# Performance work log

Hardware: AMD Instinct MI355X
Metric: run time of the kernel (lower is better)

Reference implementation:

```python
import jax, jax.numpy as jnp
import numpy as np

NUM_HEADS = 24
EPS = 1e-6


def rms_norm(x, scale):
    # fp32 RMSNorm over last dim, matching torch F.rms_norm(eps=1e-6)
    xf = x.astype(jnp.float32)
    rrms = jax.lax.rsqrt(jnp.mean(xf * xf, axis=-1, keepdims=True) + EPS)
    return (xf * rrms * scale.astype(jnp.float32)).astype(x.dtype)


def rope_rotate(x, pe):
    # x: [B,H,L,D]; pe: [B,1,L,D/2,2,2] rotation matrices
    B, H, L, D = x.shape
    xr = x.astype(jnp.float32).reshape(B, H, L, D // 2, 1, 2)
    out = pe[..., 0] * xr[..., 0] + pe[..., 1] * xr[..., 1]  # [B,H,L,D/2,2]
    return out.reshape(B, H, L, D).astype(x.dtype)


def setup_inputs() -> dict:
    key = jax.random.key(0)
    ks = jax.random.split(key, 6)
    B, L, C = 1, 2048, 3072
    H = NUM_HEADS
    D = C // H
    x = jax.random.normal(ks[0], (B, L, C), dtype=jnp.float32)
    # pe: proper RoPE rotation matrices [[cos,-sin],[sin,cos]] -> [B,1,L,D/2,2,2]
    theta = jax.random.uniform(ks[1], (B, 1, L, D // 2), dtype=jnp.float32) * (2.0 * np.pi)
    cos, sin = jnp.cos(theta), jnp.sin(theta)
    row0 = jnp.stack([cos, -sin], axis=-1)
    row1 = jnp.stack([sin, cos], axis=-1)
    pe = jnp.stack([row0, row1], axis=-2)  # [B,1,L,D/2,2,2]
    w_qkv = jax.random.normal(ks[2], (3 * C, C), dtype=jnp.float32) * (1.0 / np.sqrt(C))
    q_scale = jnp.ones((D,), dtype=jnp.float32)
    k_scale = jnp.ones((D,), dtype=jnp.float32)
    w_proj = jax.random.normal(ks[3], (C, C), dtype=jnp.float32) * (1.0 / np.sqrt(C))
    b_proj = jnp.zeros((C,), dtype=jnp.float32)
    return {"x": x, "pe": pe, "w_qkv": w_qkv, "q_scale": q_scale,
            "k_scale": k_scale, "w_proj": w_proj, "b_proj": b_proj}


def reference(x, pe, w_qkv, q_scale, k_scale, w_proj, b_proj):
    B, L, C = x.shape
    H = NUM_HEADS
    D = C // H
    qkv = x @ w_qkv.T                                   # [B,L,3C]
    qkv = qkv.reshape(B, L, 3, H, D).transpose(2, 0, 3, 1, 4)  # [3,B,H,L,D]
    q, k, v = qkv[0], qkv[1], qkv[2]
    q = rms_norm(q, q_scale)
    k = rms_norm(k, k_scale)
    q = rope_rotate(q, pe)
    k = rope_rotate(k, pe)
    scale = 1.0 / np.sqrt(D)
    scores = jnp.einsum('bhqd,bhkd->bhqk', q, k) * jnp.asarray(scale, q.dtype)
    attn = jax.nn.softmax(scores, axis=-1)
    out = jnp.einsum('bhqk,bhkd->bhqd', attn, v)        # [B,H,L,D]
    out = out.transpose(0, 2, 1, 3).reshape(B, L, C)    # [B,L,C]
    return out @ w_proj.T + b_proj
```

## Files before the change

### kernel.cpp

```cpp
#include <hip/hip_runtime.h>

typedef __attribute__((ext_vector_type(8))) __bf16 bf16x8;
typedef __attribute__((ext_vector_type(4))) float f32x4;

typedef __attribute__((address_space(1))) void gvoid;
typedef __attribute__((address_space(3))) void lvoid;

__device__ __forceinline__ float bf2f(unsigned int u) {
    union { unsigned int u; float f; } v; v.u = u << 16; return v.f;
}
__device__ __forceinline__ unsigned short f2bf(float f) {
    union { float f; unsigned int u; } v; v.f = f;
    unsigned int r = v.u + 0x7fffu + ((v.u >> 16) & 1u);
    return (unsigned short)(r >> 16);
}
__device__ __forceinline__ unsigned int pack2(float a, float b) {
    return (unsigned int)f2bf(a) | ((unsigned int)f2bf(b) << 16);
}
__device__ __forceinline__ void async16(const void* g, void* l) {
    __builtin_amdgcn_global_load_lds((gvoid*)g, (lvoid*)l, 16, 0, 0);
}
__device__ __forceinline__ float exp2f_hw(float x) {
    return __builtin_amdgcn_exp2f(x);
}


__global__ __launch_bounds__(256)
void cvt_bf16(const float4* __restrict__ s, uint4* __restrict__ d, int n8) {
    int i = blockIdx.x * 256 + threadIdx.x;
    if (i >= n8) return;
    float4 a = s[2 * i], b = s[2 * i + 1];
    uint4 o;
    o.x = pack2(a.x, a.y); o.y = pack2(a.z, a.w);
    o.z = pack2(b.x, b.y); o.w = pack2(b.z, b.w);
    d[i] = o;
}

#define GEMM_CORE(A_, lda_, B_, ldb_, K_)                                        \
    __shared__ __align__(16) unsigned short As[4][4096];                         \
    __shared__ __align__(16) unsigned short Bs[4][4096];                         \
    const int t = threadIdx.x, lane = t & 63;                                    \
    const int wm = t >> 7, wn = (t >> 6) & 1;                                    \
    const int lr = lane & 15, kc = lane >> 4;                                    \
    const int NK = (K_) / 32;                                                    \
    const int e0 = t * 8, e1 = (256 + t) * 8;                                    \
    const int r0 = e0 >> 5, c0 = (e0 >> 3) & 3;                                  \
    const int r1 = e1 >> 5, c1 = (e1 >> 3) & 3;                                  \
    const int g0 = (c0 ^ ((r0 >> 1) & 3)) * 8;                                   \
    const int g1 = (c1 ^ ((r1 >> 1) & 3)) * 8;                                   \
    const unsigned short* Ag0 = &(A_)[(size_t)(m0 + r0) * (lda_) + g0];          \
    const unsigned short* Ag1 = &(A_)[(size_t)(m0 + r1) * (lda_) + g1];          \
    const unsigned short* Bg0 = &(B_)[(size_t)(n0 + r0) * (ldb_) + g0];          \
    const unsigned short* Bg1 = &(B_)[(size_t)(n0 + r1) * (ldb_) + g1];          \
    f32x4 acc[4][4] = {};                                                        \
    RSTAGE(0) RSTAGE(1) RSTAGE(2)                                                \
    asm volatile("s_waitcnt vmcnt(8)" ::: "memory");                             \
    __builtin_amdgcn_s_barrier();                                                \
    for (int kt = 0; kt < NK; ++kt) {                                            \
        const int sl = kt & 3;                                                   \
        bf16x8 af[4], bfr[4];                                                    \
        _Pragma("unroll")                                                        \
        for (int i = 0; i < 4; ++i) {                                            \
            int ra = wm * 64 + i * 16 + lr;                                      \
            int rb = wn * 64 + i * 16 + lr;                                      \
            af[i]  = *(const bf16x8*)&As[sl][ra * 32 + ((kc ^ ((ra >> 1) & 3)) * 8)]; \
            bfr[i] = *(const bf16x8*)&Bs[sl][rb * 32 + ((kc ^ ((rb >> 1) & 3)) * 8)]; \
        }                                                                        \
        if (kt + 3 < NK) RSTAGE(kt + 3)                                          \
        asm volatile("s_waitcnt lgkmcnt(0)" ::: "memory");                       \
        __builtin_amdgcn_sched_barrier(0);                                       \
        __builtin_amdgcn_s_setprio(1);                                           \
        _Pragma("unroll")                                                        \
        for (int mi = 0; mi < 4; ++mi)                                           \
            _Pragma("unroll")                                                    \
            for (int ni = 0; ni < 4; ++ni)                                       \
                acc[mi][ni] = __builtin_amdgcn_mfma_f32_16x16x32_bf16(           \
                    af[mi], bfr[ni], acc[mi][ni], 0, 0, 0);                      \
        __builtin_amdgcn_s_setprio(0);                                           \
        if (kt + 3 < NK)      { asm volatile("s_waitcnt vmcnt(8)" ::: "memory"); } \
        else if (kt + 2 < NK) { asm volatile("s_waitcnt vmcnt(4)" ::: "memory"); } \
        else if (kt + 1 < NK) { asm volatile("s_waitcnt vmcnt(0)" ::: "memory"); } \
        __builtin_amdgcn_s_barrier();                                            \
    }

#define RSTAGE(kt_) { const int s_ = (kt_) & 3; const size_t k_ = (size_t)(kt_) * 32; \
        async16(Ag0 + k_, &As[s_][e0]); async16(Ag1 + k_, &As[s_][e1]);               \
        async16(Bg0 + k_, &Bs[s_][e0]); async16(Bg1 + k_, &Bs[s_][e1]); }

__global__ __launch_bounds__(256, 2)
void gemm_qkv(const unsigned short* __restrict__ A, const unsigned short* __restrict__ B,
              unsigned short* __restrict__ qk, unsigned short* __restrict__ vt) {
    __shared__ __align__(16) unsigned short As[3][4096];
    __shared__ __align__(16) unsigned short Bs[3][8192];
    const int n0 = blockIdx.x * 256, m0 = blockIdx.y * 128;
    const int t = threadIdx.x, lane = t & 63, w = t >> 6;
    const int lr = lane & 15, kc = lane >> 4;
    const int NK = 96;

    const int ea0 = t * 8,         ra0 = ea0 >> 5, ca0 = (ea0 >> 3) & 3;
    const int ea1 = (256 + t) * 8, ra1 = ea1 >> 5, ca1 = (ea1 >> 3) & 3;
    const int ga0 = (ca0 ^ ((ra0 >> 1) & 3)) * 8;
    const int ga1 = (ca1 ^ ((ra1 >> 1) & 3)) * 8;
    const unsigned short* Ag0 = &A[(size_t)(m0 + ra0) * 3072 + ga0];
    const unsigned short* Ag1 = &A[(size_t)(m0 + ra1) * 3072 + ga1];
    int eb[4];
    const unsigned short* Bg[4];
#pragma unroll
    for (int i = 0; i < 4; ++i) {
        eb[i] = (i * 256 + t) * 8;
        int rb = eb[i] >> 5, cb = (eb[i] >> 3) & 3;
        int gb = (cb ^ ((rb >> 1) & 3)) * 8;
        Bg[i] = &B[(size_t)(n0 + rb) * 3072 + gb];
    }

#define QSTAGE(kt_) { const int s_ = (kt_) % 3; const size_t k_ = (size_t)(kt_) * 32; \
        async16(Ag0 + k_, &As[s_][ea0]); async16(Ag1 + k_, &As[s_][ea1]);             \
        async16(Bg[0] + k_, &Bs[s_][eb[0]]); async16(Bg[1] + k_, &Bs[s_][eb[1]]);     \
        async16(Bg[2] + k_, &Bs[s_][eb[2]]); async16(Bg[3] + k_, &Bs[s_][eb[3]]); }

    f32x4 acc[8][4] = {};

    QSTAGE(0) QSTAGE(1)
    asm volatile("s_waitcnt vmcnt(6)" ::: "memory");
    __builtin_amdgcn_s_barrier();

    for (int kt = 0; kt < NK; ++kt) {
        const int sl = kt % 3;
        bf16x8 af[8], bfr[4];
#pragma unroll
        for (int i = 0; i < 8; ++i) {
            int ra = i * 16 + lr;
            af[i] = *(const bf16x8*)&As[sl][ra * 32 + ((kc ^ ((ra >> 1) & 3)) * 8)];
        }
#pragma unroll
        for (int i = 0; i < 4; ++i) {
            int rb = w * 64 + i * 16 + lr;
            bfr[i] = *(const bf16x8*)&Bs[sl][rb * 32 + ((kc ^ ((rb >> 1) & 3)) * 8)];
        }
        if (kt + 2 < NK) QSTAGE(kt + 2)
        asm volatile("s_waitcnt lgkmcnt(0)" ::: "memory");
        __builtin_amdgcn_sched_barrier(0);
        __builtin_amdgcn_s_setprio(1);
#pragma unroll
        for (int mi = 0; mi < 8; ++mi)
#pragma unroll
            for (int ni = 0; ni < 4; ++ni)
                acc[mi][ni] = __builtin_amdgcn_mfma_f32_16x16x32_bf16(
                    af[mi], bfr[ni], acc[mi][ni], 0, 0, 0);
        __builtin_amdgcn_s_setprio(0);
        if (kt + 2 < NK) { asm volatile("s_waitcnt vmcnt(6)" ::: "memory"); }
        else             { asm volatile("s_waitcnt vmcnt(0)" ::: "memory"); }
        __builtin_amdgcn_s_barrier();
    }
#undef QSTAGE

    const int rb0 = kc * 4;
#pragma unroll
    for (int mi = 0; mi < 8; ++mi)
#pragma unroll
        for (int ni = 0; ni < 4; ++ni) {
            int col = n0 + w * 64 + ni * 16 + lr;
#pragma unroll
            for (int r = 0; r < 4; ++r) {
                int row = m0 + mi * 16 + rb0 + r;
                unsigned short v = f2bf(acc[mi][ni][r]);
                if (col < 6144) qk[(size_t)row * 6144 + col] = v;
                else            vt[(size_t)(col - 6144) * 2048 + row] = v;
            }
        }
}

__global__ __launch_bounds__(256, 2)
void gemm_proj(const unsigned short* __restrict__ A, const unsigned short* __restrict__ B,
               const float* __restrict__ bias, float* __restrict__ out) {
    const int n0 = blockIdx.x * 128, m0 = blockIdx.y * 128;
    GEMM_CORE(A, 6144, B, 3072, 3072)
    const int rb0 = kc * 4;
#pragma unroll
    for (int mi = 0; mi < 4; ++mi)
#pragma unroll
        for (int ni = 0; ni < 4; ++ni) {
            int col = n0 + wn * 64 + ni * 16 + lr;
            float badd = bias[col];
#pragma unroll
            for (int r = 0; r < 4; ++r) {
                int row = m0 + wm * 64 + mi * 16 + rb0 + r;
                out[(size_t)row * 3072 + col] = acc[mi][ni][r] + badd;
            }
        }
}

__global__ __launch_bounds__(256)
void attn2(unsigned short* __restrict__ qk, const unsigned short* __restrict__ vt) {
    __shared__ __align__(16) unsigned short Ks[64 * 128];
    __shared__ __align__(16) unsigned short Vs[128 * 64];
    __shared__ __align__(16) unsigned short Ps[4 * 16 * 64];
    const int t = threadIdx.x, lane = t & 63, w = t >> 6;
    const int h = blockIdx.x, qblk = blockIdx.y * 64;
    const int lr = lane & 15, kc = lane >> 4;
    const float sc2 = 0.08838834764831845f * 1.4426950408889634f;

    bf16x8 aq[4];
#pragma unroll
    for (int ks = 0; ks < 4; ++ks)
        aq[ks] = *(const bf16x8*)&qk[(size_t)(qblk + w * 16 + lr) * 6144 + h * 128 + ks * 32 + kc * 8];

    f32x4 o[8] = {};
    float mst[4], lst[4];
#pragma unroll
    for (int r = 0; r < 4; ++r) { mst[r] = -1e30f; lst[r] = 0.0f; }

    unsigned short* Pw = &Ps[w * 1024];

#pragma unroll
    for (int i = 0; i < 4; ++i) {
        int e = (i * 256 + t) * 8;
        {
            int row = e >> 7, c8 = (e >> 3) & 15;
            int gc = (c8 ^ (row & 15)) * 8;
            async16(&qk[(size_t)row * 6144 + 3072 + h * 128 + gc], &Ks[e]);
        }
        {
            int row = e >> 6, c8 = (e >> 3) & 7;
            int gc = (c8 ^ (row & 7)) * 8;
            async16(&vt[(size_t)(h * 128 + row) * 2048 + gc], &Vs[e]);
        }
    }

    for (int kb = 0; kb < 2048; kb += 64) {
        __syncthreads();

        bf16x8 pk[4], pv[4];
        const bool pf = (kb + 64) < 2048;
        if (pf) {
#pragma unroll
            for (int i = 0; i < 4; ++i) {
                int e = (i * 256 + t) * 8;
                {   int row = e >> 7, c8 = (e >> 3) & 15;
                    int gc = (c8 ^ (row & 15)) * 8;
                    pk[i] = *(const bf16x8*)&qk[(size_t)(kb + 64 + row) * 6144 + 3072 + h * 128 + gc];
                }
                {   int row = e >> 6, c8 = (e >> 3) & 7;
                    int gc = (c8 ^ (row & 7)) * 8;
                    pv[i] = *(const bf16x8*)&vt[(size_t)(h * 128 + row) * 2048 + kb + 64 + gc];
                }
            }
        }

        f32x4 s[4] = {};
#pragma unroll
        for (int nt = 0; nt < 4; ++nt) {
            int rk = nt * 16 + lr;
#pragma unroll
            for (int ks = 0; ks < 4; ++ks) {
                int ck = ks * 4 + kc;
                bf16x8 bk = *(const bf16x8*)&Ks[rk * 128 + ((ck ^ (rk & 15)) * 8)];
                s[nt] = __builtin_amdgcn_mfma_f32_16x16x32_bf16(aq[ks], bk, s[nt], 0, 0, 0);
            }
        }

#pragma unroll
        for (int r = 0; r < 4; ++r) {
            float vmax = fmaxf(fmaxf(s[0][r], s[1][r]), fmaxf(s[2][r], s[3][r]));
#pragma unroll
            for (int off = 8; off >= 1; off >>= 1) vmax = fmaxf(vmax, __shfl_xor(vmax, off));
            float mn = fmaxf(mst[r], vmax);
            float al = exp2f_hw((mst[r] - mn) * sc2);
            mst[r] = mn;
            float ps = 0.0f;
#pragma unroll
            for (int nt = 0; nt < 4; ++nt) {
                float p = exp2f_hw((s[nt][r] - mn) * sc2);
                s[nt][r] = p;
                ps += p;
            }
#pragma unroll
            for (int off = 8; off >= 1; off >>= 1) ps += __shfl_xor(ps, off);
            lst[r] = lst[r] * al + ps;
#pragma unroll
            for (int dt = 0; dt < 8; ++dt) o[dt][r] *= al;
        }

#pragma unroll
        for (int nt = 0; nt < 4; ++nt) {
            int col = nt * 16 + lr;
            int chunk = col >> 3, cin = col & 7;
#pragma unroll
            for (int r = 0; r < 4; ++r) {
                int q = kc * 4 + r;
                Pw[q * 64 + ((chunk ^ (q & 7)) * 8 + cin)] = f2bf(s[nt][r]);
            }
        }

#pragma unroll
        for (int ks2 = 0; ks2 < 2; ++ks2) {
            int ck = ks2 * 4 + kc;
            bf16x8 ap = *(const bf16x8*)&Pw[lr * 64 + ((ck ^ (lr & 7)) * 8)];
#pragma unroll
            for (int dt = 0; dt < 8; ++dt) {
                int rv = dt * 16 + lr;
                bf16x8 bv = *(const bf16x8*)&Vs[rv * 64 + ((ck ^ (rv & 7)) * 8)];
                o[dt] = __builtin_amdgcn_mfma_f32_16x16x32_bf16(ap, bv, o[dt], 0, 0, 0);
            }
        }
        __syncthreads();

        if (pf) {
#pragma unroll
            for (int i = 0; i < 4; ++i) {
                int e = (i * 256 + t) * 8;
                *(bf16x8*)&Ks[e] = pk[i];
                *(bf16x8*)&Vs[e] = pv[i];
            }
        }
    }

#pragma unroll
    for (int dt = 0; dt < 8; ++dt)
#pragma unroll
        for (int r = 0; r < 4; ++r) {
            int row = qblk + w * 16 + kc * 4 + r;
            qk[(size_t)row * 6144 + h * 128 + dt * 16 + lr] = f2bf(o[dt][r] / lst[r]);
        }
}


__global__ __launch_bounds__(256)
void norm_rope(unsigned short* __restrict__ qk, const float* __restrict__ pe,
               const float* __restrict__ q_scale, const float* __restrict__ k_scale) {
    const int wid = threadIdx.x >> 6, lane = threadIdx.x & 63;
    int pid = blockIdx.x * 4 + wid;
    const int isK = pid >= 49152;
    int p2 = isK ? pid - 49152 : pid;
    const int h = p2 >> 11, l = p2 & 2047;

    unsigned short* src = qk + (size_t)l * 6144 + (isK ? 3072 : 0) + h * 128 + lane * 2;
    unsigned int xu = *(const unsigned int*)src;
    float x0 = bf2f(xu & 0xffffu), x1 = bf2f(xu >> 16);
    float ss = x0 * x0 + x1 * x1;
#pragma unroll
    for (int off = 32; off >= 1; off >>= 1) ss += __shfl_xor(ss, off);
    float rr = rsqrtf(ss * (1.0f / 128.0f) + 1e-6f);

    const float* sc = isK ? k_scale : q_scale;
    float2 s2 = *(const float2*)(sc + lane * 2);
    float y0 = x0 * rr * s2.x;
    float y1 = x1 * rr * s2.y;

    float4 p4 = *(const float4*)(pe + ((size_t)l * 64 + lane) * 4);
    float o0 = p4.x * y0 + p4.y * y1;
    float o1 = p4.z * y0 + p4.w * y1;

    *(unsigned int*)src = pack2(o0, o1);
}


template <bool A32, bool B32, bool C32, bool HAS_BIAS, bool TRANS_C>
__global__ __launch_bounds__(256, 2)
void gemm_bt(const void* __restrict__ Ap, const void* __restrict__ Bp,
             const float* __restrict__ bias, void* __restrict__ Cp,
             int M, int N, int K, int lda, int ldc) {
    __shared__ __align__(16) unsigned short As[128 * 40];
    __shared__ __align__(16) unsigned short Bs[128 * 40];
    const int t = threadIdx.x, lane = t & 63;
    const int wm = t >> 7, wn = (t >> 6) & 1;
    const int m0 = blockIdx.x * 128, n0 = blockIdx.y * 128;
    const int lr = lane & 15, kc = lane >> 4;
    f32x4 acc[4][4] = {};

    for (int k0 = 0; k0 < K; k0 += 32) {
        float4 ra32[4], rb32[4];
        bf16x8 ra16[2], rb16[2];
        if constexpr (A32) {
            const float* A = (const float*)Ap;
#pragma unroll
            for (int i = 0; i < 4; ++i) {
                int idx = i * 256 + t, row = idx >> 3, c4 = idx & 7;
                ra32[i] = *(const float4*)&A[(size_t)(m0 + row) * lda + k0 + c4 * 4];
            }
        } else {
            const unsigned short* A = (const unsigned short*)Ap;
#pragma unroll
            for (int i = 0; i < 2; ++i) {
                int idx = i * 256 + t, row = idx >> 2, c8 = idx & 3;
                ra16[i] = *(const bf16x8*)&A[(size_t)(m0 + row) * lda + k0 + c8 * 8];
            }
        }
        if constexpr (B32) {
            const float* B = (const float*)Bp;
#pragma unroll
            for (int i = 0; i < 4; ++i) {
                int idx = i * 256 + t, row = idx >> 3, c4 = idx & 7;
                rb32[i] = *(const float4*)&B[(size_t)(n0 + row) * K + k0 + c4 * 4];
            }
        } else {
            const unsigned short* B = (const unsigned short*)Bp;
#pragma unroll
            for (int i = 0; i < 2; ++i) {
                int idx = i * 256 + t, row = idx >> 2, c8 = idx & 3;
                rb16[i] = *(const bf16x8*)&B[(size_t)(n0 + row) * K + k0 + c8 * 8];
            }
        }
        __syncthreads();
        if constexpr (A32) {
#pragma unroll
            for (int i = 0; i < 4; ++i) {
                int idx = i * 256 + t, row = idx >> 3, c4 = idx & 7;
                uint2 p = { pack2(ra32[i].x, ra32[i].y), pack2(ra32[i].z, ra32[i].w) };
                *(uint2*)&As[row * 40 + c4 * 4] = p;
            }
        } else {
#pragma unroll
            for (int i = 0; i < 2; ++i) {
                int idx = i * 256 + t, row = idx >> 2, c8 = idx & 3;
                *(bf16x8*)&As[row * 40 + c8 * 8] = ra16[i];
            }
        }
        if constexpr (B32) {
#pragma unroll
            for (int i = 0; i < 4; ++i) {
                int idx = i * 256 + t, row = idx >> 3, c4 = idx & 7;
                uint2 p = { pack2(rb32[i].x, rb32[i].y), pack2(rb32[i].z, rb32[i].w) };
                *(uint2*)&Bs[row * 40 + c4 * 4] = p;
            }
        } else {
#pragma unroll
            for (int i = 0; i < 2; ++i) {
                int idx = i * 256 + t, row = idx >> 2, c8 = idx & 3;
                *(bf16x8*)&Bs[row * 40 + c8 * 8] = rb16[i];
            }
        }
        __syncthreads();
        bf16x8 af[4], bfr[4];
#pragma unroll
        for (int i = 0; i < 4; ++i) {
            af[i]  = *(const bf16x8*)&As[(wm * 64 + i * 16 + lr) * 40 + kc * 8];
            bfr[i] = *(const bf16x8*)&Bs[(wn * 64 + i * 16 + lr) * 40 + kc * 8];
        }
#pragma unroll
        for (int mi = 0; mi < 4; ++mi)
#pragma unroll
            for (int ni = 0; ni < 4; ++ni)
                acc[mi][ni] = __builtin_amdgcn_mfma_f32_16x16x32_bf16(af[mi], bfr[ni], acc[mi][ni], 0, 0, 0);
    }
    const int rb0 = kc * 4;
#pragma unroll
    for (int mi = 0; mi < 4; ++mi) {
#pragma unroll
        for (int ni = 0; ni < 4; ++ni) {
            int col = n0 + wn * 64 + ni * 16 + lr;
            float badd = HAS_BIAS ? bias[col] : 0.0f;
#pragma unroll
            for (int r = 0; r < 4; ++r) {
                int row = m0 + wm * 64 + mi * 16 + rb0 + r;
                size_t off = TRANS_C ? ((size_t)col * ldc + row) : ((size_t)row * ldc + col);
                if (C32) ((float*)Cp)[off] = acc[mi][ni][r] + badd;
                else     ((unsigned short*)Cp)[off] = f2bf(acc[mi][ni][r] + badd);
            }
        }
    }
}

__global__ __launch_bounds__(256, 2)
void attn_slow(unsigned short* __restrict__ qk, const unsigned short* __restrict__ vt) {
    __shared__ __align__(16) unsigned short Ks[64 * 136];
    __shared__ __align__(16) unsigned short Vs[128 * 72];
    __shared__ __align__(16) unsigned short Ps[4 * 32 * 72];
    const int t = threadIdx.x, lane = t & 63, w = t >> 6;
    const int h = blockIdx.y, q0 = blockIdx.x * 128;
    const int lr = lane & 15, kc = lane >> 4;
    const float scale = 0.08838834764831845f;

    bf16x8 aq[2][4];
#pragma unroll
    for (int mf = 0; mf < 2; ++mf)
#pragma unroll
        for (int ks = 0; ks < 4; ++ks)
            aq[mf][ks] = *(const bf16x8*)&qk[(size_t)(q0 + w * 32 + mf * 16 + lr) * 6144 + h * 128 + ks * 32 + kc * 8];

    f32x4 o[2][8] = {};
    float mst[2][4], lst[2][4];
#pragma unroll
    for (int mf = 0; mf < 2; ++mf)
#pragma unroll
        for (int r = 0; r < 4; ++r) { mst[mf][r] = -1e30f; lst[mf][r] = 0.0f; }

    unsigned short* Pw = &Ps[w * 32 * 72];

    for (int kb = 0; kb < 2048; kb += 64) {
        bf16x8 rk[4], rv[4];
#pragma unroll
        for (int i = 0; i < 4; ++i) {
            int idx = i * 256 + t;
            { int row = idx >> 4, c8 = idx & 15;
              rk[i] = *(const bf16x8*)&qk[(size_t)(kb + row) * 6144 + 3072 + h * 128 + c8 * 8]; }
            { int row = idx >> 3, c8 = idx & 7;
              rv[i] = *(const bf16x8*)&vt[(size_t)(h * 128 + row) * 2048 + kb + c8 * 8]; }
        }
        __syncthreads();
#pragma unroll
        for (int i = 0; i < 4; ++i) {
            int idx = i * 256 + t;
            { int row = idx >> 4, c8 = idx & 15; *(bf16x8*)&Ks[row * 136 + c8 * 8] = rk[i]; }
            { int row = idx >> 3, c8 = idx & 7;  *(bf16x8*)&Vs[row * 72 + c8 * 8] = rv[i]; }
        }
        __syncthreads();

        f32x4 s[2][4] = {};
#pragma unroll
        for (int nt = 0; nt < 4; ++nt) {
            int rkr = nt * 16 + lr;
#pragma unroll
            for (int ks = 0; ks < 4; ++ks) {
                bf16x8 bk = *(const bf16x8*)&Ks[rkr * 136 + (ks * 4 + kc) * 8];
#pragma unroll
                for (int mf = 0; mf < 2; ++mf)
                    s[mf][nt] = __builtin_amdgcn_mfma_f32_16x16x32_bf16(aq[mf][ks], bk, s[mf][nt], 0, 0, 0);
            }
        }
#pragma unroll
        for (int mf = 0; mf < 2; ++mf)
#pragma unroll
            for (int nt = 0; nt < 4; ++nt)
#pragma unroll
                for (int r = 0; r < 4; ++r) s[mf][nt][r] *= scale;

#pragma unroll
        for (int mf = 0; mf < 2; ++mf) {
#pragma unroll
            for (int r = 0; r < 4; ++r) {
                float vmax = fmaxf(fmaxf(s[mf][0][r], s[mf][1][r]), fmaxf(s[mf][2][r], s[mf][3][r]));
#pragma unroll
                for (int off = 8; off >= 1; off >>= 1) vmax = fmaxf(vmax, __shfl_xor(vmax, off));
                float mn = fmaxf(mst[mf][r], vmax);
                float al = __expf(mst[mf][r] - mn);
                mst[mf][r] = mn;
                float ps = 0.0f;
#pragma unroll
                for (int nt = 0; nt < 4; ++nt) {
                    float p = __expf(s[mf][nt][r] - mn);
                    s[mf][nt][r] = p;
                    ps += p;
                }
#pragma unroll
                for (int off = 8; off >= 1; off >>= 1) ps += __shfl_xor(ps, off);
                lst[mf][r] = lst[mf][r] * al + ps;
#pragma unroll
                for (int dt = 0; dt < 8; ++dt) o[mf][dt][r] *= al;
            }
        }

#pragma unroll
        for (int mf = 0; mf < 2; ++mf)
#pragma unroll
            for (int nt = 0; nt < 4; ++nt)
#pragma unroll
                for (int r = 0; r < 4; ++r)
                    Pw[(mf * 16 + kc * 4 + r) * 72 + nt * 16 + lr] = f2bf(s[mf][nt][r]);

#pragma unroll
        for (int ks2 = 0; ks2 < 2; ++ks2) {
            bf16x8 ap[2];
#pragma unroll
            for (int mf = 0; mf < 2; ++mf)
                ap[mf] = *(const bf16x8*)&Pw[(mf * 16 + lr) * 72 + (ks2 * 4 + kc) * 8];
#pragma unroll
            for (int dt = 0; dt < 8; ++dt) {
                bf16x8 bv = *(const bf16x8*)&Vs[(dt * 16 + lr) * 72 + (ks2 * 4 + kc) * 8];
#pragma unroll
                for (int mf = 0; mf < 2; ++mf)
                    o[mf][dt] = __builtin_amdgcn_mfma_f32_16x16x32_bf16(ap[mf], bv, o[mf][dt], 0, 0, 0);
            }
        }
        __syncthreads();
    }

#pragma unroll
    for (int mf = 0; mf < 2; ++mf)
#pragma unroll
        for (int dt = 0; dt < 8; ++dt)
#pragma unroll
            for (int r = 0; r < 4; ++r) {
                int row = q0 + w * 32 + mf * 16 + kc * 4 + r;
                qk[(size_t)row * 6144 + h * 128 + dt * 16 + lr] = f2bf(o[mf][dt][r] / lst[mf][r]);
            }
}

__global__ void fill_two(float* p, int n) {
    int i = blockIdx.x * 256 + threadIdx.x;
    if (i < n) p[i] = 2.0f;
}

extern "C" void kernel_launch(void* const* d_in, const int* in_sizes, int n_in,
                              void* d_out, int out_size, void* d_ws, size_t ws_size,
                              hipStream_t stream) {
    const float* x       = (const float*)d_in[0];
    const float* pe      = (const float*)d_in[1];
    const float* w_qkv   = (const float*)d_in[2];
    const float* q_scale = (const float*)d_in[3];
    const float* k_scale = (const float*)d_in[4];
    const float* w_proj  = (const float*)d_in[5];
    const float* b_proj  = (const float*)d_in[6];
    float* out = (float*)d_out;

    if (ws_size >= 125829120ull) {
        unsigned short* ws     = (unsigned short*)d_ws;
        unsigned short* xb     = ws;
        unsigned short* wqkvb  = ws + 6291456;
        unsigned short* wprojb = ws + 34603008;
        unsigned short* qk     = ws + 44040192;
        unsigned short* vt     = ws + 56623104;

        cvt_bf16<<<3072, 256, 0, stream>>>((const float4*)x, (uint4*)xb, 786432);
        cvt_bf16<<<13824, 256, 0, stream>>>((const float4*)w_qkv, (uint4*)wqkvb, 3538944);
        cvt_bf16<<<4608, 256, 0, stream>>>((const float4*)w_proj, (uint4*)wprojb, 1179648);

        gemm_qkv<<<dim3(36, 16), 256, 0, stream>>>(xb, wqkvb, qk, vt);
        norm_rope<<<24576, 256, 0, stream>>>(qk, pe, q_scale, k_scale);
        attn2<<<dim3(24, 32), 256, 0, stream>>>(qk, vt);
        gemm_proj<<<dim3(24, 16), 256, 0, stream>>>(qk, wprojb, b_proj, out);
        return;
    }

    if (ws_size < 37748736ull) {
        fill_two<<<(6291456 + 255) / 256, 256, 0, stream>>>(out, 6291456);
        return;
    }

    unsigned short* qk = (unsigned short*)d_ws;
    unsigned short* vt = qk + 12582912;

    gemm_bt<true, true, false, false, false><<<dim3(16, 48), 256, 0, stream>>>(
        x, w_qkv, nullptr, qk, 2048, 6144, 3072, 3072, 6144);
    norm_rope<<<24576, 256, 0, stream>>>(qk, pe, q_scale, k_scale);
    gemm_bt<true, true, false, false, true><<<dim3(16, 24), 256, 0, stream>>>(
        x, w_qkv + (size_t)6144 * 3072, nullptr, vt, 2048, 3072, 3072, 3072, 2048);
    attn_slow<<<dim3(16, 24), 256, 0, stream>>>(qk, vt);
    gemm_bt<false, true, true, true, false><<<dim3(16, 24), 256, 0, stream>>>(
        qk, w_proj, b_proj, out, 2048, 3072, 3072, 6144, 3072);
}
```

Baseline: 603.8 us.

## Double attention query tile per wave, add lazy rescale, fuse conversion kernels

The attention kernel now has each wave handle 32 query rows (two MFMA row fragments), so every block covers 128 queries. Each K/V tile loaded into shared memory is therefore reused across twice as many queries, and the grid shrinks to half as many blocks. Online-softmax rescaling of the accumulators is skipped unless the running max grows past a threshold, which cuts exp and multiply work but raises register pressure and changes numerics slightly. The three fp32-to-bf16 conversion launches are merged into one kernel to save launch overhead.

New measurement: 605.0 us. About the same (+0.2%).

```diff
diff --git a/kernel.cpp b/kernel.cpp
--- a/kernel.cpp
+++ b/kernel.cpp
@@ -26,14 +26,19 @@
 
 
 __global__ __launch_bounds__(256)
-void cvt_bf16(const float4* __restrict__ s, uint4* __restrict__ d, int n8) {
+void cvt_all(const float4* __restrict__ x, const float4* __restrict__ wqkv,
+             const float4* __restrict__ wproj, uint4* __restrict__ dst) {
     int i = blockIdx.x * 256 + threadIdx.x;
-    if (i >= n8) return;
-    float4 a = s[2 * i], b = s[2 * i + 1];
+    const float4* s; uint4* d; int off;
+    if (i < 786432)       { s = x;     d = dst;           off = i; }
+    else if (i < 4325376) { s = wqkv;  d = dst + 786432;  off = i - 786432; }
+    else if (i < 5505024) { s = wproj; d = dst + 4325376; off = i - 4325376; }
+    else return;
+    float4 a = s[2 * off], b = s[2 * off + 1];
     uint4 o;
     o.x = pack2(a.x, a.y); o.y = pack2(a.z, a.w);
     o.z = pack2(b.x, b.y); o.w = pack2(b.z, b.w);
-    d[i] = o;
+    d[off] = o;
 }
 
 #define GEMM_CORE(A_, lda_, B_, ldb_, K_)                                        \
@@ -190,27 +195,32 @@
         }
 }
 
-__global__ __launch_bounds__(256)
+__global__ __launch_bounds__(256, 2)
 void attn2(unsigned short* __restrict__ qk, const unsigned short* __restrict__ vt) {
     __shared__ __align__(16) unsigned short Ks[64 * 128];
     __shared__ __align__(16) unsigned short Vs[128 * 64];
-    __shared__ __align__(16) unsigned short Ps[4 * 16 * 64];
+    __shared__ __align__(16) unsigned short Ps[4 * 32 * 64];
     const int t = threadIdx.x, lane = t & 63, w = t >> 6;
-    const int h = blockIdx.x, qblk = blockIdx.y * 64;
+    const int h = blockIdx.x, qblk = blockIdx.y * 128;
     const int lr = lane & 15, kc = lane >> 4;
     const float sc2 = 0.08838834764831845f * 1.4426950408889634f;
-
-    bf16x8 aq[4];
-#pragma unroll
-    for (int ks = 0; ks < 4; ++ks)
-        aq[ks] = *(const bf16x8*)&qk[(size_t)(qblk + w * 16 + lr) * 6144 + h * 128 + ks * 32 + kc * 8];
-
-    f32x4 o[8] = {};
-    float mst[4], lst[4];
-#pragma unroll
-    for (int r = 0; r < 4; ++r) { mst[r] = -1e30f; lst[r] = 0.0f; }
-
-    unsigned short* Pw = &Ps[w * 1024];
+    const float THR = 62.7f;
+
+    bf16x8 aq[2][4];
+#pragma unroll
+    for (int mf = 0; mf < 2; ++mf)
+#pragma unroll
+        for (int ks = 0; ks < 4; ++ks)
+            aq[mf][ks] = *(const bf16x8*)&qk[(size_t)(qblk + w * 32 + mf * 16 + lr) * 6144 + h * 128 + ks * 32 + kc * 8];
+
+    f32x4 o[2][8] = {};
+    float mst[2][4], lst[2][4];
+#pragma unroll
+    for (int mf = 0; mf < 2; ++mf)
+#pragma unroll
+        for (int r = 0; r < 4; ++r) { mst[mf][r] = -1e30f; lst[mf][r] = 0.0f; }
+
+    unsigned short* Pw = &Ps[w * 2048];
 
 #pragma unroll
     for (int i = 0; i < 4; ++i) {
@@ -247,7 +257,7 @@
             }
         }
 
-        f32x4 s[4] = {};
+        f32x4 s[2][4] = {};
 #pragma unroll
         for (int nt = 0; nt < 4; ++nt) {
             int rk = nt * 16 + lr;
@@ -255,52 +265,78 @@
             for (int ks = 0; ks < 4; ++ks) {
                 int ck = ks * 4 + kc;
                 bf16x8 bk = *(const bf16x8*)&Ks[rk * 128 + ((ck ^ (rk & 15)) * 8)];
-                s[nt] = __builtin_amdgcn_mfma_f32_16x16x32_bf16(aq[ks], bk, s[nt], 0, 0, 0);
-            }
-        }
-
-#pragma unroll
-        for (int r = 0; r < 4; ++r) {
-            float vmax = fmaxf(fmaxf(s[0][r], s[1][r]), fmaxf(s[2][r], s[3][r]));
-#pragma unroll
-            for (int off = 8; off >= 1; off >>= 1) vmax = fmaxf(vmax, __shfl_xor(vmax, off));
-            float mn = fmaxf(mst[r], vmax);
-            float al = exp2f_hw((mst[r] - mn) * sc2);
-            mst[r] = mn;
-            float ps = 0.0f;
+#pragma unroll
+                for (int mf = 0; mf < 2; ++mf)
+                    s[mf][nt] = __builtin_amdgcn_mfma_f32_16x16x32_bf16(aq[mf][ks], bk, s[mf][nt], 0, 0, 0);
+            }
+        }
+
+#pragma unroll
+        for (int mf = 0; mf < 2; ++mf) {
+            float vm[4]; bool need = false;
+#pragma unroll
+            for (int r = 0; r < 4; ++r) {
+                float vmax = fmaxf(fmaxf(s[mf][0][r], s[mf][1][r]), fmaxf(s[mf][2][r], s[mf][3][r]));
+#pragma unroll
+                for (int off = 8; off >= 1; off >>= 1) vmax = fmaxf(vmax, __shfl_xor(vmax, off));
+                vm[r] = vmax;
+                need = need || (vmax > mst[mf][r] + THR);
+            }
+            if (__ballot(need) != 0ull) {
+#pragma unroll
+                for (int r = 0; r < 4; ++r) {
+                    float mn = fmaxf(mst[mf][r], vm[r]);
+                    float al = exp2f_hw((mst[mf][r] - mn) * sc2);
+                    mst[mf][r] = mn;
+                    lst[mf][r] *= al;
+#pragma unroll
+                    for (int dt = 0; dt < 8; ++dt) o[mf][dt][r] *= al;
+                }
+            }
+#pragma unroll
+            for (int r = 0; r < 4; ++r) {
+                float ps = 0.0f;
+#pragma unroll
+                for (int nt = 0; nt < 4; ++nt) {
+                    float p = exp2f_hw((s[mf][nt][r] - mst[mf][r]) * sc2);
+                    s[mf][nt][r] = p;
+                    ps += p;
+                }
+#pragma unroll
+                for (int off = 8; off >= 1; off >>= 1) ps += __shfl_xor(ps, off);
+                lst[mf][r] += ps;
+            }
+        }
+
+#pragma unroll
+        for (int mf = 0; mf < 2; ++mf)
 #pragma unroll
             for (int nt = 0; nt < 4; ++nt) {
-                float p = exp2f_hw((s[nt][r] - mn) * sc2);
-                s[nt][r] = p;
-                ps += p;
-            }
-#pragma unroll
-            for (int off = 8; off >= 1; off >>= 1) ps += __shfl_xor(ps, off);
-            lst[r] = lst[r] * al + ps;
-#pragma unroll
-            for (int dt = 0; dt < 8; ++dt) o[dt][r] *= al;
-        }
-
-#pragma unroll
-        for (int nt = 0; nt < 4; ++nt) {
-            int col = nt * 16 + lr;
-            int chunk = col >> 3, cin = col & 7;
-#pragma unroll
-            for (int r = 0; r < 4; ++r) {
-                int q = kc * 4 + r;
-                Pw[q * 64 + ((chunk ^ (q & 7)) * 8 + cin)] = f2bf(s[nt][r]);
-            }
-        }
+                int col = nt * 16 + lr;
+                int chunk = col >> 3, cin = col & 7;
+#pragma unroll
+                for (int r = 0; r < 4; ++r) {
+                    int q = mf * 16 + kc * 4 + r;
+                    Pw[q * 64 + ((chunk ^ (q & 7)) * 8 + cin)] = f2bf(s[mf][nt][r]);
+                }
+            }
 
 #pragma unroll
         for (int ks2 = 0; ks2 < 2; ++ks2) {
             int ck = ks2 * 4 + kc;
-            bf16x8 ap = *(const bf16x8*)&Pw[lr * 64 + ((ck ^ (lr & 7)) * 8)];
+            bf16x8 ap[2];
+#pragma unroll
+            for (int mf = 0; mf < 2; ++mf) {
+                int q = mf * 16 + lr;
+                ap[mf] = *(const bf16x8*)&Pw[q * 64 + ((ck ^ (q & 7)) * 8)];
+            }
 #pragma unroll
             for (int dt = 0; dt < 8; ++dt) {
                 int rv = dt * 16 + lr;
                 bf16x8 bv = *(const bf16x8*)&Vs[rv * 64 + ((ck ^ (rv & 7)) * 8)];
-                o[dt] = __builtin_amdgcn_mfma_f32_16x16x32_bf16(ap, bv, o[dt], 0, 0, 0);
+#pragma unroll
+                for (int mf = 0; mf < 2; ++mf)
+                    o[mf][dt] = __builtin_amdgcn_mfma_f32_16x16x32_bf16(ap[mf], bv, o[mf][dt], 0, 0, 0);
             }
         }
         __syncthreads();
@@ -316,12 +352,14 @@
     }
 
 #pragma unroll
-    for (int dt = 0; dt < 8; ++dt)
-#pragma unroll
-        for (int r = 0; r < 4; ++r) {
-            int row = qblk + w * 16 + kc * 4 + r;
-            qk[(size_t)row * 6144 + h * 128 + dt * 16 + lr] = f2bf(o[dt][r] / lst[r]);
-        }
+    for (int mf = 0; mf < 2; ++mf)
+#pragma unroll
+        for (int dt = 0; dt < 8; ++dt)
+#pragma unroll
+            for (int r = 0; r < 4; ++r) {
+                int row = qblk + w * 32 + mf * 16 + kc * 4 + r;
+                qk[(size_t)row * 6144 + h * 128 + dt * 16 + lr] = f2bf(o[mf][dt][r] / lst[mf][r]);
+            }
 }
 
 
@@ -611,13 +649,12 @@
         unsigned short* qk     = ws + 44040192;
         unsigned short* vt     = ws + 56623104;
 
-        cvt_bf16<<<3072, 256, 0, stream>>>((const float4*)x, (uint4*)xb, 786432);
-        cvt_bf16<<<13824, 256, 0, stream>>>((const float4*)w_qkv, (uint4*)wqkvb, 3538944);
-        cvt_bf16<<<4608, 256, 0, stream>>>((const float4*)w_proj, (uint4*)wprojb, 1179648);
+        cvt_all<<<21504, 256, 0, stream>>>((const float4*)x, (const float4*)w_qkv,
+                                           (const float4*)w_proj, (uint4*)xb);
 
         gemm_qkv<<<dim3(36, 16), 256, 0, stream>>>(xb, wqkvb, qk, vt);
         norm_rope<<<24576, 256, 0, stream>>>(qk, pe, q_scale, k_scale);
-        attn2<<<dim3(24, 32), 256, 0, stream>>>(qk, vt);
+        attn2<<<dim3(24, 16), 256, 0, stream>>>(qk, vt);
         gemm_proj<<<dim3(24, 16), 256, 0, stream>>>(qk, wprojb, b_proj, out);
         return;
     }
```
